# Kernel tuning notes

Hardware: AMD Instinct MI355X
Metric: run time of the kernel (lower is better)

Reference implementation:

```python
import jax, jax.numpy as jnp
import numpy as np

EPS = 1e-12

def _l2norm(v, axis):
    # matches torch F.normalize: divide by norm clamped to eps
    n = jnp.sqrt(jnp.sum(v * v, axis=axis, keepdims=True))
    return v / jnp.maximum(n, EPS)

def setup_inputs() -> dict:
    key = jax.random.key(0)
    k1, k2 = jax.random.split(key)
    B, C, S, D = 256, 1000, 4, 512
    x = jax.random.normal(k1, (B, D), dtype=jnp.float32)
    # xavier_uniform over [C, S, D]: fan_in = S*D? torch treats dims (S, D) pairwise; approximate with uniform bound
    bound = float(np.sqrt(6.0 / (S + D)))
    W = jax.random.uniform(k2, (C, S, D), dtype=jnp.float32, minval=-bound, maxval=bound)
    return {"x": x, "W": W}

def reference(x, W):
    xn = _l2norm(x, axis=1)            # [B, D]
    Wn = _l2norm(W, axis=2)            # [C, S, D]
    logits = jnp.einsum('bd,csd->bcs', xn, Wn)        # [B, C, S]
    x_proj = jnp.einsum('bcs,csd->bcd', logits, Wn)   # [B, C, D]
    x_proj = _l2norm(x_proj, axis=2)
    out = jnp.einsum('bd,bcd->bc', xn, x_proj)        # [B, C]
    return out
```

## Files before the change

### kernel.cpp

```cpp
#include <hip/hip_runtime.h>

#define B_ 256
#define C_ 1000
#define D_ 512

typedef __bf16 bf16x4 __attribute__((ext_vector_type(4)));
typedef __bf16 bf16x8 __attribute__((ext_vector_type(8)));
typedef float  f32x4  __attribute__((ext_vector_type(4)));

__device__ __forceinline__ bf16x8 cvt8(float4 a, float4 b) {
    bf16x8 r;
    r[0] = (__bf16)a.x; r[1] = (__bf16)a.y; r[2] = (__bf16)a.z; r[3] = (__bf16)a.w;
    r[4] = (__bf16)b.x; r[5] = (__bf16)b.y; r[6] = (__bf16)b.z; r[7] = (__bf16)b.w;
    return r;
}
__device__ __forceinline__ bf16x4 cvt4(float4 a) {
    bf16x4 r;
    r[0] = (__bf16)a.x; r[1] = (__bf16)a.y; r[2] = (__bf16)a.z; r[3] = (__bf16)a.w;
    return r;
}

__global__ __launch_bounds__(256) void k_packx(const float* __restrict__ x,
                                               __bf16* __restrict__ xf,
                                               float* __restrict__ invx) {
    int n = blockIdx.x * 256 + threadIdx.x;
    int r = n >> 6;
    int j = n & 63;
    const float* src = x + r * D_ + j * 8;
    float4 a = *(const float4*)src;
    float4 b = *(const float4*)(src + 4);
    int bt = r >> 4, l15 = r & 15, ks = j >> 2, quad = j & 3;
    int idx = ((bt * 16 + ks) * 4 + quad) * 16 + l15;
    *(bf16x8*)(xf + idx * 8) = cvt8(a, b);
    float sn = a.x*a.x + a.y*a.y + a.z*a.z + a.w*a.w
             + b.x*b.x + b.y*b.y + b.z*b.z + b.w*b.w;
    #pragma unroll
    for (int o = 32; o; o >>= 1) sn += __shfl_down(sn, o);
    if ((threadIdx.x & 63) == 0) invx[r] = 1.0f / fmaxf(sqrtf(sn), 1e-12f);
}

__global__ __launch_bounds__(256, 2) void k_main(const float* __restrict__ W,
                                                 const __bf16* __restrict__ xf,
                                                 const float* __restrict__ invx,
                                                 float* __restrict__ out) {
    __shared__ __align__(16) char smem[64 * 272];
    int blk = blockIdx.x;
    int ct = blk >> 1;
    int bh = blk & 1;
    int t = threadIdx.x;
    int lane = t & 63, wv = t >> 6;
    int l15 = lane & 15, quad = lane >> 4;

    const float* wbase = W + ct * 16 * D_;
    #pragma unroll
    for (int p = 0; p < 8; p++) {
        int ch = t + 256 * p;
        int row = ch >> 7, pos = ch & 127;
        float4 v = *(const float4*)(wbase + row * D_ + pos * 4);
        int ks = pos >> 3, qd = (pos >> 1) & 3, off = (pos & 1) * 4;
        *(bf16x4*)(smem + (ks * 4 + qd) * 272 + row * 16 + off * 2) = cvt4(v);
    }
    __syncthreads();

    int bt0 = bh * 8 + wv * 2;
    int bt1 = bt0 + 1;
    const bf16x8* xp0 = (const bf16x8*)xf + (bt0 * 64 + quad) * 16 + l15;
    const bf16x8* xp1 = (const bf16x8*)xf + (bt1 * 64 + quad) * 16 + l15;
    const char* lp = smem + quad * 272 + l15 * 16;

    f32x4 acc0 = {0.f, 0.f, 0.f, 0.f};
    f32x4 acc1 = {0.f, 0.f, 0.f, 0.f};
    f32x4 accg = {0.f, 0.f, 0.f, 0.f};
    #pragma unroll
    for (int ks = 0; ks < 16; ks++) {
        bf16x8 af = *(const bf16x8*)(lp + ks * 1088);
        bf16x8 b0 = xp0[ks * 64];
        bf16x8 b1 = xp1[ks * 64];
        acc0 = __builtin_amdgcn_mfma_f32_16x16x32_bf16(af, b0, acc0, 0, 0, 0);
        acc1 = __builtin_amdgcn_mfma_f32_16x16x32_bf16(af, b1, acc1, 0, 0, 0);
        accg = __builtin_amdgcn_mfma_f32_16x16x32_bf16(af, af, accg, 0, 0, 0);
    }

    float g[4][4];
    #pragma unroll
    for (int s = 0; s < 4; s++) {
        float v = accg[s];
        #pragma unroll
        for (int q = 0; q < 4; q++) g[s][q] = __shfl(v, 20 * quad + q);
    }
    float iv[4];
    #pragma unroll
    for (int s = 0; s < 4; s++) iv[s] = 1.0f / fmaxf(sqrtf(fmaxf(g[s][s], 0.f)), 1e-12f);

    #pragma unroll
    for (int sub = 0; sub < 2; sub++) {
        int bt = sub ? bt1 : bt0;
        f32x4 acc = sub ? acc1 : acc0;
        float ivx = invx[bt * 16 + l15];
        float l[4];
        #pragma unroll
        for (int s = 0; s < 4; s++) l[s] = acc[s] * ivx * iv[s];
        float num = l[0]*l[0] + l[1]*l[1] + l[2]*l[2] + l[3]*l[3];
        float den2 = 0.f;
        #pragma unroll
        for (int s = 0; s < 4; s++) {
            float r = 0.f;
            #pragma unroll
            for (int q = 0; q < 4; q++) r += g[s][q] * iv[q] * l[q];
            den2 += l[s] * iv[s] * r;
        }
        float den = fmaxf(sqrtf(fmaxf(den2, 0.f)), 1e-12f);
        float val = num / den;

        float4 o;
        o.x = __shfl(val, l15);
        o.y = __shfl(val, l15 + 16);
        o.z = __shfl(val, l15 + 32);
        o.w = __shfl(val, l15 + 48);
        if (quad == 0)
            *(float4*)(out + (bt * 16 + l15) * C_ + ct * 4) = o;
    }
}

extern "C" void kernel_launch(void* const* d_in, const int* in_sizes, int n_in,
                              void* d_out, int out_size, void* d_ws, size_t ws_size,
                              hipStream_t stream) {
    const float* x = (const float*)d_in[0];
    const float* W = (const float*)d_in[1];
    float* out = (float*)d_out;

    char* ws = (char*)d_ws;
    __bf16* xf  = (__bf16*)ws;
    float*  ivx = (float*)(ws + 524288);

    k_packx<<<64, 256, 0, stream>>>(x, xf, ivx);
    k_main<<<500, 256, 0, stream>>>(W, xf, ivx, out);
}
```

Measured before the change: 69.16 us.

## Fuse x packing and norm into main kernel, dropping pack launch

```diff
diff --git a/kernel.cpp b/kernel.cpp
--- a/kernel.cpp
+++ b/kernel.cpp
@@ -20,29 +20,9 @@
     return r;
 }
 
-__global__ __launch_bounds__(256) void k_packx(const float* __restrict__ x,
-                                               __bf16* __restrict__ xf,
-                                               float* __restrict__ invx) {
-    int n = blockIdx.x * 256 + threadIdx.x;
-    int r = n >> 6;
-    int j = n & 63;
-    const float* src = x + r * D_ + j * 8;
-    float4 a = *(const float4*)src;
-    float4 b = *(const float4*)(src + 4);
-    int bt = r >> 4, l15 = r & 15, ks = j >> 2, quad = j & 3;
-    int idx = ((bt * 16 + ks) * 4 + quad) * 16 + l15;
-    *(bf16x8*)(xf + idx * 8) = cvt8(a, b);
-    float sn = a.x*a.x + a.y*a.y + a.z*a.z + a.w*a.w
-             + b.x*b.x + b.y*b.y + b.z*b.z + b.w*b.w;
-    #pragma unroll
-    for (int o = 32; o; o >>= 1) sn += __shfl_down(sn, o);
-    if ((threadIdx.x & 63) == 0) invx[r] = 1.0f / fmaxf(sqrtf(sn), 1e-12f);
-}
-
-__global__ __launch_bounds__(256, 2) void k_main(const float* __restrict__ W,
-                                                 const __bf16* __restrict__ xf,
-                                                 const float* __restrict__ invx,
-                                                 float* __restrict__ out) {
+__global__ __launch_bounds__(256, 2) void k_fused(const float* __restrict__ x,
+                                                  const float* __restrict__ W,
+                                                  float* __restrict__ out) {
     __shared__ __align__(16) char smem[64 * 272];
     int blk = blockIdx.x;
     int ct = blk >> 1;
@@ -64,22 +44,36 @@
 
     int bt0 = bh * 8 + wv * 2;
     int bt1 = bt0 + 1;
-    const bf16x8* xp0 = (const bf16x8*)xf + (bt0 * 64 + quad) * 16 + l15;
-    const bf16x8* xp1 = (const bf16x8*)xf + (bt1 * 64 + quad) * 16 + l15;
+    const float* xr0 = x + (bt0 * 16 + l15) * D_ + quad * 8;
+    const float* xr1 = x + (bt1 * 16 + l15) * D_ + quad * 8;
     const char* lp = smem + quad * 272 + l15 * 16;
 
     f32x4 acc0 = {0.f, 0.f, 0.f, 0.f};
     f32x4 acc1 = {0.f, 0.f, 0.f, 0.f};
     f32x4 accg = {0.f, 0.f, 0.f, 0.f};
+    float sn0 = 0.f, sn1 = 0.f;
     #pragma unroll
     for (int ks = 0; ks < 16; ks++) {
+        float4 a0 = *(const float4*)(xr0 + ks * 32);
+        float4 c0 = *(const float4*)(xr0 + ks * 32 + 4);
+        float4 a1 = *(const float4*)(xr1 + ks * 32);
+        float4 c1 = *(const float4*)(xr1 + ks * 32 + 4);
         bf16x8 af = *(const bf16x8*)(lp + ks * 1088);
-        bf16x8 b0 = xp0[ks * 64];
-        bf16x8 b1 = xp1[ks * 64];
+        bf16x8 b0 = cvt8(a0, c0);
+        bf16x8 b1 = cvt8(a1, c1);
+        sn0 += a0.x*a0.x + a0.y*a0.y + a0.z*a0.z + a0.w*a0.w
+             + c0.x*c0.x + c0.y*c0.y + c0.z*c0.z + c0.w*c0.w;
+        sn1 += a1.x*a1.x + a1.y*a1.y + a1.z*a1.z + a1.w*a1.w
+             + c1.x*c1.x + c1.y*c1.y + c1.z*c1.z + c1.w*c1.w;
         acc0 = __builtin_amdgcn_mfma_f32_16x16x32_bf16(af, b0, acc0, 0, 0, 0);
         acc1 = __builtin_amdgcn_mfma_f32_16x16x32_bf16(af, b1, acc1, 0, 0, 0);
         accg = __builtin_amdgcn_mfma_f32_16x16x32_bf16(af, af, accg, 0, 0, 0);
     }
+
+    sn0 += __shfl_xor(sn0, 16); sn0 += __shfl_xor(sn0, 32);
+    sn1 += __shfl_xor(sn1, 16); sn1 += __shfl_xor(sn1, 32);
+    float ivx0 = 1.0f / fmaxf(sqrtf(sn0), 1e-12f);
+    float ivx1 = 1.0f / fmaxf(sqrtf(sn1), 1e-12f);
 
     float g[4][4];
     #pragma unroll
@@ -96,7 +90,7 @@
     for (int sub = 0; sub < 2; sub++) {
         int bt = sub ? bt1 : bt0;
         f32x4 acc = sub ? acc1 : acc0;
-        float ivx = invx[bt * 16 + l15];
+        float ivx = sub ? ivx1 : ivx0;
         float l[4];
         #pragma unroll
         for (int s = 0; s < 4; s++) l[s] = acc[s] * ivx * iv[s];
@@ -128,11 +122,5 @@
     const float* x = (const float*)d_in[0];
     const float* W = (const float*)d_in[1];
     float* out = (float*)d_out;
-
-    char* ws = (char*)d_ws;
-    __bf16* xf  = (__bf16*)ws;
-    float*  ivx = (float*)(ws + 524288);
-
-    k_packx<<<64, 256, 0, stream>>>(x, xf, ivx);
-    k_main<<<500, 256, 0, stream>>>(W, xf, ivx, out);
+    k_fused<<<500, 256, 0, stream>>>(x, W, out);
 }
```

New measurement: 78.55 us. 1.14x slower.

## Process two class tiles per block to reuse x fragments

Applied to the files above, without the earlier changes.

```diff
diff --git a/kernel.cpp b/kernel.cpp
--- a/kernel.cpp
+++ b/kernel.cpp
@@ -43,82 +43,94 @@
                                                  const __bf16* __restrict__ xf,
                                                  const float* __restrict__ invx,
                                                  float* __restrict__ out) {
-    __shared__ __align__(16) char smem[64 * 272];
+    __shared__ __align__(16) char smW[2 * 64 * 272];
     int blk = blockIdx.x;
-    int ct = blk >> 1;
+    int ct2 = blk >> 1;
     int bh = blk & 1;
     int t = threadIdx.x;
     int lane = t & 63, wv = t >> 6;
     int l15 = lane & 15, quad = lane >> 4;
 
-    const float* wbase = W + ct * 16 * D_;
+    const float* wbase = W + ct2 * 32 * D_;
     #pragma unroll
-    for (int p = 0; p < 8; p++) {
+    for (int p = 0; p < 16; p++) {
         int ch = t + 256 * p;
         int row = ch >> 7, pos = ch & 127;
         float4 v = *(const float4*)(wbase + row * D_ + pos * 4);
         int ks = pos >> 3, qd = (pos >> 1) & 3, off = (pos & 1) * 4;
-        *(bf16x4*)(smem + (ks * 4 + qd) * 272 + row * 16 + off * 2) = cvt4(v);
+        *(bf16x4*)(smW + (row >> 4) * 17408 + (ks * 4 + qd) * 272
+                       + (row & 15) * 16 + off * 2) = cvt4(v);
     }
     __syncthreads();
 
-    int bt0 = bh * 8 + wv * 2;
-    int bt1 = bt0 + 1;
+    int bt0 = bh * 8 + wv * 2, bt1 = bt0 + 1;
     const bf16x8* xp0 = (const bf16x8*)xf + (bt0 * 64 + quad) * 16 + l15;
     const bf16x8* xp1 = (const bf16x8*)xf + (bt1 * 64 + quad) * 16 + l15;
-    const char* lp = smem + quad * 272 + l15 * 16;
+    const char* lp0 = smW + quad * 272 + l15 * 16;
+    const char* lp1 = lp0 + 17408;
 
-    f32x4 acc0 = {0.f, 0.f, 0.f, 0.f};
-    f32x4 acc1 = {0.f, 0.f, 0.f, 0.f};
-    f32x4 accg = {0.f, 0.f, 0.f, 0.f};
+    f32x4 acc00 = {0.f,0.f,0.f,0.f}, acc01 = {0.f,0.f,0.f,0.f};
+    f32x4 acc10 = {0.f,0.f,0.f,0.f}, acc11 = {0.f,0.f,0.f,0.f};
+    f32x4 accg0 = {0.f,0.f,0.f,0.f}, accg1 = {0.f,0.f,0.f,0.f};
     #pragma unroll
     for (int ks = 0; ks < 16; ks++) {
-        bf16x8 af = *(const bf16x8*)(lp + ks * 1088);
+        bf16x8 a0 = *(const bf16x8*)(lp0 + ks * 1088);
+        bf16x8 a1 = *(const bf16x8*)(lp1 + ks * 1088);
         bf16x8 b0 = xp0[ks * 64];
         bf16x8 b1 = xp1[ks * 64];
-        acc0 = __builtin_amdgcn_mfma_f32_16x16x32_bf16(af, b0, acc0, 0, 0, 0);
-        acc1 = __builtin_amdgcn_mfma_f32_16x16x32_bf16(af, b1, acc1, 0, 0, 0);
-        accg = __builtin_amdgcn_mfma_f32_16x16x32_bf16(af, af, accg, 0, 0, 0);
+        acc00 = __builtin_amdgcn_mfma_f32_16x16x32_bf16(a0, b0, acc00, 0, 0, 0);
+        acc01 = __builtin_amdgcn_mfma_f32_16x16x32_bf16(a0, b1, acc01, 0, 0, 0);
+        acc10 = __builtin_amdgcn_mfma_f32_16x16x32_bf16(a1, b0, acc10, 0, 0, 0);
+        acc11 = __builtin_amdgcn_mfma_f32_16x16x32_bf16(a1, b1, acc11, 0, 0, 0);
+        accg0 = __builtin_amdgcn_mfma_f32_16x16x32_bf16(a0, a0, accg0, 0, 0, 0);
+        accg1 = __builtin_amdgcn_mfma_f32_16x16x32_bf16(a1, a1, accg1, 0, 0, 0);
     }
 
-    float g[4][4];
-    #pragma unroll
-    for (int s = 0; s < 4; s++) {
-        float v = accg[s];
-        #pragma unroll
-        for (int q = 0; q < 4; q++) g[s][q] = __shfl(v, 20 * quad + q);
-    }
-    float iv[4];
-    #pragma unroll
-    for (int s = 0; s < 4; s++) iv[s] = 1.0f / fmaxf(sqrtf(fmaxf(g[s][s], 0.f)), 1e-12f);
+    float ivx0 = invx[bt0 * 16 + l15];
+    float ivx1 = invx[bt1 * 16 + l15];
 
     #pragma unroll
-    for (int sub = 0; sub < 2; sub++) {
-        int bt = sub ? bt1 : bt0;
-        f32x4 acc = sub ? acc1 : acc0;
-        float ivx = invx[bt * 16 + l15];
-        float l[4];
-        #pragma unroll
-        for (int s = 0; s < 4; s++) l[s] = acc[s] * ivx * iv[s];
-        float num = l[0]*l[0] + l[1]*l[1] + l[2]*l[2] + l[3]*l[3];
-        float den2 = 0.f;
+    for (int u = 0; u < 2; u++) {
+        f32x4 accg = u ? accg1 : accg0;
+        float g[4][4];
         #pragma unroll
         for (int s = 0; s < 4; s++) {
-            float r = 0.f;
+            float v = accg[s];
             #pragma unroll
-            for (int q = 0; q < 4; q++) r += g[s][q] * iv[q] * l[q];
-            den2 += l[s] * iv[s] * r;
+            for (int q = 0; q < 4; q++) g[s][q] = __shfl(v, 20 * quad + q);
         }
-        float den = fmaxf(sqrtf(fmaxf(den2, 0.f)), 1e-12f);
-        float val = num / den;
+        float iv[4];
+        #pragma unroll
+        for (int s = 0; s < 4; s++) iv[s] = 1.0f / fmaxf(sqrtf(fmaxf(g[s][s], 0.f)), 1e-12f);
 
-        float4 o;
-        o.x = __shfl(val, l15);
-        o.y = __shfl(val, l15 + 16);
-        o.z = __shfl(val, l15 + 32);
-        o.w = __shfl(val, l15 + 48);
-        if (quad == 0)
-            *(float4*)(out + (bt * 16 + l15) * C_ + ct * 4) = o;
+        #pragma unroll
+        for (int sub = 0; sub < 2; sub++) {
+            f32x4 acc = u ? (sub ? acc11 : acc10) : (sub ? acc01 : acc00);
+            float ivx = sub ? ivx1 : ivx0;
+            int bt = sub ? bt1 : bt0;
+            float l[4];
+            #pragma unroll
+            for (int s = 0; s < 4; s++) l[s] = acc[s] * ivx * iv[s];
+            float num = l[0]*l[0] + l[1]*l[1] + l[2]*l[2] + l[3]*l[3];
+            float den2 = 0.f;
+            #pragma unroll
+            for (int s = 0; s < 4; s++) {
+                float r = 0.f;
+                #pragma unroll
+                for (int q = 0; q < 4; q++) r += g[s][q] * iv[q] * l[q];
+                den2 += l[s] * iv[s] * r;
+            }
+            float den = fmaxf(sqrtf(fmaxf(den2, 0.f)), 1e-12f);
+            float val = num / den;
+
+            float4 o;
+            o.x = __shfl(val, l15);
+            o.y = __shfl(val, l15 + 16);
+            o.z = __shfl(val, l15 + 32);
+            o.w = __shfl(val, l15 + 48);
+            if (quad == 0)
+                *(float4*)(out + (bt * 16 + l15) * C_ + ct2 * 8 + u * 4) = o;
+        }
     }
 }
 
@@ -134,5 +146,5 @@
     float*  ivx = (float*)(ws + 524288);
 
     k_packx<<<64, 256, 0, stream>>>(x, xf, ivx);
-    k_main<<<500, 256, 0, stream>>>(W, xf, ivx, out);
+    k_main<<<250, 256, 0, stream>>>(W, xf, ivx, out);
 }
```

After: 69.16 us. No clear change (+0.0%).
